# Kernel tuning notes

Measured on AMD Instinct MI355X. Metric: run time of the kernel, lower is better.

## Reference

```python
import jax, jax.numpy as jnp
import numpy as np

PI = float(np.pi)


def _m2(a, b, c, d):
    a, b, c, d = [jnp.asarray(x, jnp.complex64) for x in (a, b, c, d)]
    return jnp.stack([jnp.stack([a, b]), jnp.stack([c, d])])


def _rx(t):
    c, s = jnp.cos(t / 2), jnp.sin(t / 2)
    return _m2(c, -1j * s, -1j * s, c)


def _ry(t):
    c, s = jnp.cos(t / 2), jnp.sin(t / 2)
    return _m2(c, -s, s, c)


def _rz(t):
    e = jnp.exp(-0.5j * t)
    return _m2(e, 0.0, 0.0, jnp.conj(e))


def _rot(phi, theta, omega):
    # PennyLane Rot = RZ(omega) RY(theta) RZ(phi)
    return _rz(omega) @ _ry(theta) @ _rz(phi)


def _cgate(U):
    return jnp.eye(4, dtype=jnp.complex64).at[2:, 2:].set(U)


def _apply(state, U, wires):
    # state: [B] + [2]*8, U: [2^k, 2^k], wires: static wire indices
    axes = tuple(w + 1 for w in wires)
    k = len(wires)
    st = jnp.moveaxis(state, axes, tuple(range(1, 1 + k)))
    sh = st.shape
    st = jnp.einsum('ij,bjr->bir', U, st.reshape(sh[0], 2 ** k, -1))
    return jnp.moveaxis(st.reshape(sh), tuple(range(1, 1 + k)), axes)


def _mlp(x, W1, b1, W2, b2):
    return jax.nn.leaky_relu(x @ W1 + b1) @ W2 + b2


def _circuit(ang, inits, update):
    # ang: [B,7,2] = (RY,RZ) angles for wires 0..6 (edges on 0..2, nodes on 3..6); ancilla wire 7 = |0>
    a, b = ang[..., 0], ang[..., 1]
    q = jnp.stack([jnp.exp(-0.5j * b) * jnp.cos(0.5 * a),
                   jnp.exp(0.5j * b) * jnp.sin(0.5 * a)], -1).astype(jnp.complex64)  # [B,7,2]
    state = q[:, 0]
    for w in range(1, 7):
        state = jnp.einsum('b...,bk->b...k', state, q[:, w])
    state = jnp.einsum('b...,k->b...k', state, jnp.array([1.0, 0.0], jnp.complex64))  # [B]+[2]*8
    crx = _cgate(_rx(inits[0, 0]))
    cry = _cgate(_ry(inits[0, 1]))
    crz = _cgate(_rz(inits[0, 2]))
    for i in range(3):  # message_passing_pqc per edge
        state = _apply(state, crx, (4 + i, 7))
        state = _apply(state, cry, (i, 7))
        state = _apply(state, crz, (4 + i, 7))
    CNOT = jnp.array([[1, 0, 0, 0], [0, 1, 0, 0], [0, 0, 0, 1], [0, 0, 1, 0]], jnp.complex64)
    wgt = update[0]  # [L,2,3] StronglyEntanglingLayers on wires (3,7)
    for l in range(wgt.shape[0]):
        state = _apply(state, _rot(wgt[l, 0, 0], wgt[l, 0, 1], wgt[l, 0, 2]), (3,))
        state = _apply(state, _rot(wgt[l, 1, 0], wgt[l, 1, 1], wgt[l, 1, 2]), (7,))
        state = _apply(state, CNOT, (3, 7))
        state = _apply(state, CNOT, (7, 3))
    pr = state.real ** 2 + state.imag ** 2
    # probs over wires (3,7): sum out wires 0,1,2,4,5,6 -> [B,2,2] -> [B,4]
    return pr.sum(axis=(1, 2, 3, 5, 6, 7)).reshape(pr.shape[0], 4)


def setup_inputs() -> dict:
    N, DEG, NG = 32768, 3, 32
    FN, FE, H, PQC, POUT = 16, 8, 128, 2, 4
    rng = np.random.default_rng(0)
    f32 = lambda a: jnp.asarray(a, jnp.float32)
    p = lambda *s: f32(0.1 * rng.standard_normal(s))
    neighbors = rng.integers(0, N, size=(N, DEG))
    return dict(
        node_feat=f32(rng.standard_normal((N, FN))),
        edge_attr=f32(rng.standard_normal((N * DEG, FE))),
        node_W1=p(FN, H), node_b1=p(H), node_W2=p(H, PQC), node_b2=p(PQC),
        edge_W1=p(FE, H), edge_b1=p(H), edge_W2=p(H, PQC), edge_b2=p(PQC),
        inits=p(1, 3), update=p(1, 1, 2, 3),
        upd_W1=p(PQC + POUT, H), upd_b1=p(H), upd_W2=p(H, PQC), upd_b2=p(PQC),
        ln_g=jnp.ones((PQC,), jnp.float32), ln_b=jnp.zeros((PQC,), jnp.float32),
        head_W1=p(PQC, 2), head_b1=p(2), head_W2=p(2, 2), head_b2=p(2),
        sub_nodes=jnp.asarray(np.concatenate([np.arange(N)[:, None], neighbors], 1), jnp.int32),
        sub_edges=jnp.asarray(np.arange(N * DEG).reshape(N, DEG), jnp.int32),
        batch=jnp.asarray(np.arange(N) // (N // NG), jnp.int32),
    )


def reference(node_feat, edge_attr, node_W1, node_b1, node_W2, node_b2,
              edge_W1, edge_b1, edge_W2, edge_b2, inits, update,
              upd_W1, upd_b1, upd_W2, upd_b2, ln_g, ln_b,
              head_W1, head_b1, head_W2, head_b2,
              sub_nodes, sub_edges, batch):
    nf = jnp.tanh(_mlp(node_feat, node_W1, node_b1, node_W2, node_b2)) * PI  # [N,2]
    ef = jnp.tanh(_mlp(edge_attr, edge_W1, edge_b1, edge_W2, edge_b2)) * PI  # [E,2]
    ang = jnp.concatenate([ef[sub_edges], nf[sub_nodes]], axis=1)  # [N,7,2]
    probs = _circuit(ang, inits, update)  # [N,4]
    centers = sub_nodes[:, 0]
    upd = jnp.tanh(_mlp(jnp.concatenate([nf[centers], probs], 1),
                        upd_W1, upd_b1, upd_W2, upd_b2)) * PI
    updates_node = nf.at[centers].set((nf[centers] + upd) * 0.5)
    x = updates_node + nf
    mu = x.mean(-1, keepdims=True)
    var = ((x - mu) ** 2).mean(-1, keepdims=True)
    xn = (x - mu) / jnp.sqrt(var + 1e-5) * ln_g + ln_b  # LayerNorm(2)
    ng = 32
    g = jax.ops.segment_sum(xn, batch, num_segments=ng) / \
        jax.ops.segment_sum(jnp.ones_like(xn[:, :1]), batch, num_segments=ng)
    return _mlp(g, head_W1, head_b1, head_W2, head_b2)
```

## Files before the change

kernel.cpp:

```cpp
#include <hip/hip_runtime.h>
#include <math.h>

static constexpr float PI_F = 3.14159265358979323846f;


__device__ inline void rot2(float p, float t, float o, float R[2][2][2]) {
    float ct = cosf(0.5f*t), st = sinf(0.5f*t);
    float apo = 0.5f*(p+o), amo = 0.5f*(p-o);
    R[0][0][0] =  ct*cosf(apo); R[0][0][1] = -ct*sinf(apo);
    R[0][1][0] = -st*cosf(amo); R[0][1][1] = -st*sinf(amo);
    R[1][0][0] =  st*cosf(amo); R[1][0][1] = -st*sinf(amo);
    R[1][1][0] =  ct*cosf(apo); R[1][1][1] =  ct*sinf(apo);
}

__global__ __launch_bounds__(256) void k_mlp(
    const float* __restrict__ node_feat, const float* __restrict__ edge_attr,
    const float* __restrict__ nW1, const float* __restrict__ nb1,
    const float* __restrict__ nW2, const float* __restrict__ nb2,
    const float* __restrict__ eW1, const float* __restrict__ eb1,
    const float* __restrict__ eW2, const float* __restrict__ eb2,
    const float* __restrict__ inits, const float* __restrict__ update,
    float* __restrict__ ws, int N, int NE, int nbE)
{
    const int tid = threadIdx.x;
    const int blk = blockIdx.x;

    if (blk == 0) {
        if (tid < 96) ws[tid] = 0.f;
        if (tid == 96) ((int*)ws)[96] = 0;
        if (tid < 64) {
            float cx = cosf(0.5f*inits[0]), sx = sinf(0.5f*inits[0]);
            float cy = cosf(0.5f*inits[1]), sy = sinf(0.5f*inits[1]);
            float cz = cosf(0.5f*inits[2]), sz = sinf(0.5f*inits[2]);
            float v0r = 1.f, v0i = 0.f, v1r = 0.f, v1i = 0.f;
            #pragma unroll
            for (int i = 0; i < 3; ++i) {
                int xb = (tid >> (3+i)) & 1;
                int yb = (tid >> i) & 1;
                if (xb) {
                    float n0r = cx*v0r + sx*v1i, n0i = cx*v0i - sx*v1r;
                    float n1r = sx*v0i + cx*v1r, n1i = -sx*v0r + cx*v1i;
                    v0r=n0r; v0i=n0i; v1r=n1r; v1i=n1i;
                }
                if (yb) {
                    float n0r = cy*v0r - sy*v1r, n0i = cy*v0i - sy*v1i;
                    float n1r = sy*v0r + cy*v1r, n1i = sy*v0i + cy*v1i;
                    v0r=n0r; v0i=n0i; v1r=n1r; v1i=n1i;
                }
                if (xb) {
                    float n0r = cz*v0r + sz*v0i, n0i = cz*v0i - sz*v0r;
                    float n1r = cz*v1r - sz*v1i, n1i = cz*v1i + sz*v1r;
                    v0r=n0r; v0i=n0i; v1r=n1r; v1i=n1i;
                }
            }
            ws[128 + tid*4 + 0] = v0r*v0r + v0i*v0i;
            ws[128 + tid*4 + 1] = v1r*v1r + v1i*v1i;
            ws[128 + tid*4 + 2] = v0r*v1r + v0i*v1i;
            ws[128 + tid*4 + 3] = v0i*v1r - v0r*v1i;
        } else if (tid == 64) {
            float Ra[2][2][2], Rb[2][2][2];
            rot2(update[0], update[1], update[2], Ra);
            rot2(update[3], update[4], update[5], Rb);
            const int src[4] = {0, 2, 3, 1};
            #pragma unroll
            for (int k = 0; k < 4; ++k) {
                int r = src[k], r3 = r >> 1, r7 = r & 1;
                #pragma unroll
                for (int c = 0; c < 4; ++c) {
                    int c3 = c >> 1, c7 = c & 1;
                    float ar = Ra[r3][c3][0], ai = Ra[r3][c3][1];
                    float br = Rb[r7][c7][0], bi = Rb[r7][c7][1];
                    ws[384 + (k*4+c)*2 + 0] = ar*br - ai*bi;
                    ws[384 + (k*4+c)*2 + 1] = ar*bi + ai*br;
                }
            }
        }
    }

    if (blk < nbE) {
        int e = blk * 256 + tid;
        if (e >= NE) return;
        const float4* xp = (const float4*)(edge_attr + (size_t)e * 8);
        float4 v0 = xp[0], v1 = xp[1];
        float x[8] = {v0.x,v0.y,v0.z,v0.w, v1.x,v1.y,v1.z,v1.w};
        float t[128];
        #pragma unroll
        for (int h = 0; h < 128; ++h) t[h] = eb1[h];
        #pragma unroll
        for (int i = 0; i < 8; ++i) {
            const float* row = eW1 + i*128;
            float xi = x[i];
            #pragma unroll
            for (int h = 0; h < 128; ++h) t[h] = fmaf(xi, row[h], t[h]);
        }
        float acc = 0.f;
        #pragma unroll
        for (int h = 0; h < 128; ++h) {
            float lt = t[h] > 0.f ? t[h] : 0.01f * t[h];
            acc = fmaf(lt, eW2[2*h], acc);
        }
        ws[512 + 2*(size_t)N + e] = tanhf(acc + eb2[0]) * PI_F;
    } else {
        int n = (blk - nbE) * 256 + tid;
        if (n >= N) return;
        const float4* xp = (const float4*)(node_feat + (size_t)n * 16);
        float4 v0 = xp[0], v1 = xp[1], v2 = xp[2], v3 = xp[3];
        float x[16] = {v0.x,v0.y,v0.z,v0.w, v1.x,v1.y,v1.z,v1.w,
                       v2.x,v2.y,v2.z,v2.w, v3.x,v3.y,v3.z,v3.w};
        float t[128];
        #pragma unroll
        for (int h = 0; h < 128; ++h) t[h] = nb1[h];
        #pragma unroll
        for (int i = 0; i < 16; ++i) {
            const float* row = nW1 + i*128;
            float xi = x[i];
            #pragma unroll
            for (int h = 0; h < 128; ++h) t[h] = fmaf(xi, row[h], t[h]);
        }
        float a0 = 0.f, a1 = 0.f;
        #pragma unroll
        for (int h = 0; h < 128; ++h) {
            float lt = t[h] > 0.f ? t[h] : 0.01f * t[h];
            a0 = fmaf(lt, nW2[2*h],   a0);
            a1 = fmaf(lt, nW2[2*h+1], a1);
        }
        float2 o;
        o.x = tanhf(a0 + nb2[0]) * PI_F;
        o.y = tanhf(a1 + nb2[1]) * PI_F;
        ((float2*)(ws + 512))[n] = o;
    }
}

__global__ __launch_bounds__(256) void k_circ(
    float* __restrict__ ws,
    const float* __restrict__ uW1, const float* __restrict__ ub1,
    const float* __restrict__ uW2, const float* __restrict__ ub2,
    const float* __restrict__ lng, const float* __restrict__ lnb,
    const int* __restrict__ sub_nodes, const int* __restrict__ sub_edges,
    const int* __restrict__ batch,
    const float* __restrict__ hW1, const float* __restrict__ hb1,
    const float* __restrict__ hW2, const float* __restrict__ hb2,
    float* __restrict__ out, int N)
{
    const int tid = threadIdx.x;
    const float2* nf  = (const float2*)(ws + 512);
    const float* ef1  = ws + 512 + 2*(size_t)N;
    const float4* phi4 = (const float4*)(ws + 128);
    const float* U    = ws + 384;

    int n0 = blockIdx.x * 256 + tid;
    bool valid = n0 < N;
    int n = valid ? n0 : N - 1;

    const int4 sn = ((const int4*)sub_nodes)[n];
    int se0 = sub_edges[3*(size_t)n+0], se1 = sub_edges[3*(size_t)n+1], se2 = sub_edges[3*(size_t)n+2];

    float pe[3][2], pn[3][2];
    {
        float c0 = cosf(ef1[se0]), c1 = cosf(ef1[se1]), c2 = cosf(ef1[se2]);
        pe[0][0]=0.5f*(1.f+c0); pe[0][1]=0.5f*(1.f-c0);
        pe[1][0]=0.5f*(1.f+c1); pe[1][1]=0.5f*(1.f-c1);
        pe[2][0]=0.5f*(1.f+c2); pe[2][1]=0.5f*(1.f-c2);
        float d0 = cosf(nf[sn.y].x), d1 = cosf(nf[sn.z].x), d2 = cosf(nf[sn.w].x);
        pn[0][0]=0.5f*(1.f+d0); pn[0][1]=0.5f*(1.f-d0);
        pn[1][0]=0.5f*(1.f+d1); pn[1][1]=0.5f*(1.f-d1);
        pn[2][0]=0.5f*(1.f+d2); pn[2][1]=0.5f*(1.f-d2);
    }
    float E[8], Nw[8];
    #pragma unroll
    for (int m = 0; m < 8; ++m) {
        E[m]  = pe[0][m&1] * pe[1][(m>>1)&1] * pe[2][(m>>2)&1];
        Nw[m] = pn[0][m&1] * pn[1][(m>>1)&1] * pn[2][(m>>2)&1];
    }
    float S0 = 0.f, S1 = 0.f, Sr = 0.f, Si = 0.f;
    #pragma unroll
    for (int m = 0; m < 64; ++m) {
        float W = E[m & 7] * Nw[m >> 3];
        float4 g = phi4[m];
        S0 = fmaf(W, g.x, S0); S1 = fmaf(W, g.y, S1);
        Sr = fmaf(W, g.z, Sr); Si = fmaf(W, g.w, Si);
    }
    float2 nfc = nf[sn.x];
    float ca = cosf(0.5f*nfc.x), sa = sinf(0.5f*nfc.x);
    float cb = cosf(0.5f*nfc.y), sb = sinf(0.5f*nfc.y);
    float q0r = ca*cb, q0i = -ca*sb, q1r = sa*cb, q1i = sa*sb;
    float P[4];
    #pragma unroll
    for (int k = 0; k < 4; ++k) {
        float T0r, T0i, T1r, T1i;
        {
            float u0r = U[(k*4+0)*2], u0i = U[(k*4+0)*2+1];
            float u1r = U[(k*4+2)*2], u1i = U[(k*4+2)*2+1];
            T0r = u0r*q0r - u0i*q0i + u1r*q1r - u1i*q1i;
            T0i = u0r*q0i + u0i*q0r + u1r*q1i + u1i*q1r;
        }
        {
            float u0r = U[(k*4+1)*2], u0i = U[(k*4+1)*2+1];
            float u1r = U[(k*4+3)*2], u1i = U[(k*4+3)*2+1];
            T1r = u0r*q0r - u0i*q0i + u1r*q1r - u1i*q1i;
            T1i = u0r*q0i + u0i*q0r + u1r*q1i + u1i*q1r;
        }
        float Ar = T0r*T1r + T0i*T1i, Ai = T0i*T1r - T0r*T1i;
        P[k] = (T0r*T0r + T0i*T0i)*S0 + (T1r*T1r + T1i*T1i)*S1 + 2.f*(Ar*Sr - Ai*Si);
    }
    float in6[6] = {nfc.x, nfc.y, P[0], P[1], P[2], P[3]};
    float t[128];
    #pragma unroll
    for (int h = 0; h < 128; ++h) t[h] = ub1[h];
    #pragma unroll
    for (int i = 0; i < 6; ++i) {
        const float* row = uW1 + i*128;
        float xi = in6[i];
        #pragma unroll
        for (int h = 0; h < 128; ++h) t[h] = fmaf(xi, row[h], t[h]);
    }
    float u0 = 0.f, u1 = 0.f;
    #pragma unroll
    for (int h = 0; h < 128; ++h) {
        float lt = t[h] > 0.f ? t[h] : 0.01f * t[h];
        u0 = fmaf(lt, uW2[2*h],   u0);
        u1 = fmaf(lt, uW2[2*h+1], u1);
    }
    float x0 = 1.5f*nfc.x + 0.5f*(tanhf(u0 + ub2[0]) * PI_F);
    float x1 = 1.5f*nfc.y + 0.5f*(tanhf(u1 + ub2[1]) * PI_F);
    float mu = 0.5f*(x0 + x1);
    float d  = x0 - mu;
    float inv = 1.0f / sqrtf(d*d + 1e-5f);
    float wv  = valid ? 1.f : 0.f;
    float xn0 = ( d*inv*lng[0] + lnb[0]) * wv;
    float xn1 = (-d*inv*lng[1] + lnb[1]) * wv;
    int bs = batch[n];

    bool uni = __all(bs == __shfl(bs, 0));
    if (uni) {
        float r0 = xn0, r1 = xn1, rc = wv;
        #pragma unroll
        for (int off = 32; off >= 1; off >>= 1) {
            r0 += __shfl_xor(r0, off); r1 += __shfl_xor(r1, off); rc += __shfl_xor(rc, off);
        }
        if ((tid & 63) == 0) {
            atomicAdd(&ws[bs*3+0], r0);
            atomicAdd(&ws[bs*3+1], r1);
            atomicAdd(&ws[bs*3+2], rc);
        }
    } else if (valid) {
        atomicAdd(&ws[bs*3+0], xn0);
        atomicAdd(&ws[bs*3+1], xn1);
        atomicAdd(&ws[bs*3+2], 1.f);
    }

    __shared__ int sLast;
    __threadfence();
    __syncthreads();
    if (tid == 0) {
        int old = atomicAdd((int*)ws + 96, 1);
        sLast = (old == (int)gridDim.x - 1) ? 1 : 0;
    }
    __syncthreads();
    if (sLast && tid < 32) {
        float cnt = atomicAdd(&ws[tid*3+2], 0.f);
        float iv  = cnt > 0.f ? 1.f/cnt : 0.f;
        float g0  = atomicAdd(&ws[tid*3+0], 0.f) * iv;
        float g1  = atomicAdd(&ws[tid*3+1], 0.f) * iv;
        float h0, h1;
        {
            float a = hb1[0] + g0*hW1[0] + g1*hW1[2];
            float b = hb1[1] + g0*hW1[1] + g1*hW1[3];
            h0 = a > 0.f ? a : 0.01f*a;
            h1 = b > 0.f ? b : 0.01f*b;
        }
        out[tid*2+0] = hb2[0] + h0*hW2[0] + h1*hW2[2];
        out[tid*2+1] = hb2[1] + h0*hW2[1] + h1*hW2[3];
    }
}

extern "C" void kernel_launch(void* const* d_in, const int* in_sizes, int n_in,
                              void* d_out, int out_size, void* d_ws, size_t ws_size,
                              hipStream_t stream)
{
    const float* node_feat = (const float*)d_in[0];
    const float* edge_attr = (const float*)d_in[1];
    const float* node_W1 = (const float*)d_in[2];
    const float* node_b1 = (const float*)d_in[3];
    const float* node_W2 = (const float*)d_in[4];
    const float* node_b2 = (const float*)d_in[5];
    const float* edge_W1 = (const float*)d_in[6];
    const float* edge_b1 = (const float*)d_in[7];
    const float* edge_W2 = (const float*)d_in[8];
    const float* edge_b2 = (const float*)d_in[9];
    const float* inits   = (const float*)d_in[10];
    const float* update  = (const float*)d_in[11];
    const float* upd_W1  = (const float*)d_in[12];
    const float* upd_b1  = (const float*)d_in[13];
    const float* upd_W2  = (const float*)d_in[14];
    const float* upd_b2  = (const float*)d_in[15];
    const float* ln_g    = (const float*)d_in[16];
    const float* ln_b    = (const float*)d_in[17];
    const float* head_W1 = (const float*)d_in[18];
    const float* head_b1 = (const float*)d_in[19];
    const float* head_W2 = (const float*)d_in[20];
    const float* head_b2 = (const float*)d_in[21];
    const int* sub_nodes = (const int*)d_in[22];
    const int* sub_edges = (const int*)d_in[23];
    const int* batch     = (const int*)d_in[24];

    int N  = in_sizes[24];
    int NE = in_sizes[1] / 8;

    float* w = (float*)d_ws;
    size_t need = (512 + 2*(size_t)N + (size_t)NE) * sizeof(float);
    if (ws_size < need) return;

    int nbE = (NE + 255) / 256;
    int nbN = (N + 255) / 256;
    k_mlp<<<nbE + nbN, 256, 0, stream>>>(node_feat, edge_attr,
        node_W1, node_b1, node_W2, node_b2,
        edge_W1, edge_b1, edge_W2, edge_b2,
        inits, update, w, N, NE, nbE);
    k_circ<<<nbN, 256, 0, stream>>>(w,
        upd_W1, upd_b1, upd_W2, upd_b2, ln_g, ln_b,
        sub_nodes, sub_edges, batch,
        head_W1, head_b1, head_W2, head_b2,
        (float*)d_out, N);
}
```

Measured before the change: 44.43 us.

## Pre-transpose MLP weights into per-hidden-unit rows and loop over hidden units

Adds a prep kernel that repacks the node, edge and update MLP weights into per-hidden-unit rows with the bias and output weights interleaved. Each MLP is then computed one hidden unit at a time using float4 loads, so the 128-float register array of hidden activations is no longer needed. The intent is lower register pressure, better occupancy and fewer scalar loads. The cost is an extra kernel launch on the serial path and a larger workspace.

```diff
diff --git a/kernel.cpp b/kernel.cpp
--- a/kernel.cpp
+++ b/kernel.cpp
@@ -3,6 +3,10 @@
 
 static constexpr float PI_F = 3.14159265358979323846f;
 
+#define WS_NT 448
+#define WS_ET 3008
+#define WS_UT 4544
+#define WS_NF 6144
 
 __device__ inline void rot2(float p, float t, float o, float R[2][2][2]) {
     float ct = cosf(0.5f*t), st = sinf(0.5f*t);
@@ -13,128 +17,149 @@
     R[1][1][0] =  ct*cosf(apo); R[1][1][1] =  ct*sinf(apo);
 }
 
+__global__ __launch_bounds__(256) void k_prep(
+    const float* __restrict__ nW1, const float* __restrict__ nb1, const float* __restrict__ nW2,
+    const float* __restrict__ eW1, const float* __restrict__ eb1, const float* __restrict__ eW2,
+    const float* __restrict__ uW1, const float* __restrict__ ub1, const float* __restrict__ uW2,
+    const float* __restrict__ inits, const float* __restrict__ update,
+    float* __restrict__ ws)
+{
+    const int tid = threadIdx.x;
+    if (tid < 96) ws[tid] = 0.f;
+    if (tid == 96) ((int*)ws)[96] = 0;
+
+    if (tid < 64) {
+        float cx = cosf(0.5f*inits[0]), sx = sinf(0.5f*inits[0]);
+        float cy = cosf(0.5f*inits[1]), sy = sinf(0.5f*inits[1]);
+        float cz = cosf(0.5f*inits[2]), sz = sinf(0.5f*inits[2]);
+        float v0r = 1.f, v0i = 0.f, v1r = 0.f, v1i = 0.f;
+        #pragma unroll
+        for (int i = 0; i < 3; ++i) {
+            int xb = (tid >> (3+i)) & 1;
+            int yb = (tid >> i) & 1;
+            if (xb) {
+                float n0r = cx*v0r + sx*v1i, n0i = cx*v0i - sx*v1r;
+                float n1r = sx*v0i + cx*v1r, n1i = -sx*v0r + cx*v1i;
+                v0r=n0r; v0i=n0i; v1r=n1r; v1i=n1i;
+            }
+            if (yb) {
+                float n0r = cy*v0r - sy*v1r, n0i = cy*v0i - sy*v1i;
+                float n1r = sy*v0r + cy*v1r, n1i = sy*v0i + cy*v1i;
+                v0r=n0r; v0i=n0i; v1r=n1r; v1i=n1i;
+            }
+            if (xb) {
+                float n0r = cz*v0r + sz*v0i, n0i = cz*v0i - sz*v0r;
+                float n1r = cz*v1r - sz*v1i, n1i = cz*v1i + sz*v1r;
+                v0r=n0r; v0i=n0i; v1r=n1r; v1i=n1i;
+            }
+        }
+        ws[128 + tid*4 + 0] = v0r*v0r + v0i*v0i;
+        ws[128 + tid*4 + 1] = v1r*v1r + v1i*v1i;
+        ws[128 + tid*4 + 2] = v0r*v1r + v0i*v1i;
+        ws[128 + tid*4 + 3] = v0i*v1r - v0r*v1i;
+    } else if (tid == 64) {
+        float Ra[2][2][2], Rb[2][2][2];
+        rot2(update[0], update[1], update[2], Ra);
+        rot2(update[3], update[4], update[5], Rb);
+        const int src[4] = {0, 2, 3, 1};
+        #pragma unroll
+        for (int k = 0; k < 4; ++k) {
+            int r = src[k], r3 = r >> 1, r7 = r & 1;
+            #pragma unroll
+            for (int c = 0; c < 4; ++c) {
+                int c3 = c >> 1, c7 = c & 1;
+                float ar = Ra[r3][c3][0], ai = Ra[r3][c3][1];
+                float br = Rb[r7][c7][0], bi = Rb[r7][c7][1];
+                ws[384 + (k*4+c)*2 + 0] = ar*br - ai*bi;
+                ws[384 + (k*4+c)*2 + 1] = ar*bi + ai*br;
+            }
+        }
+    }
+
+    if (tid < 128) {
+        int h = tid;
+        float* r = ws + WS_NT + h*20;
+        #pragma unroll
+        for (int i = 0; i < 16; ++i) r[i] = nW1[i*128 + h];
+        r[16] = nb1[h]; r[17] = nW2[2*h]; r[18] = nW2[2*h+1]; r[19] = 0.f;
+    } else {
+        int h = tid - 128;
+        float* re = ws + WS_ET + h*12;
+        #pragma unroll
+        for (int i = 0; i < 8; ++i) re[i] = eW1[i*128 + h];
+        re[8] = eb1[h]; re[9] = eW2[2*h]; re[10] = 0.f; re[11] = 0.f;
+        float* ru = ws + WS_UT + h*12;
+        #pragma unroll
+        for (int i = 0; i < 6; ++i) ru[i] = uW1[i*128 + h];
+        ru[6] = ub1[h]; ru[7] = uW2[2*h]; ru[8] = uW2[2*h+1];
+        ru[9] = 0.f; ru[10] = 0.f; ru[11] = 0.f;
+    }
+}
+
 __global__ __launch_bounds__(256) void k_mlp(
     const float* __restrict__ node_feat, const float* __restrict__ edge_attr,
-    const float* __restrict__ nW1, const float* __restrict__ nb1,
-    const float* __restrict__ nW2, const float* __restrict__ nb2,
-    const float* __restrict__ eW1, const float* __restrict__ eb1,
-    const float* __restrict__ eW2, const float* __restrict__ eb2,
-    const float* __restrict__ inits, const float* __restrict__ update,
-    float* __restrict__ ws, int N, int NE, int nbE)
+    const float* __restrict__ nT, const float* __restrict__ eT,
+    const float* __restrict__ nb2, const float* __restrict__ eb2,
+    float2* __restrict__ nf, float* __restrict__ ef1,
+    int N, int NE, int nbE)
 {
     const int tid = threadIdx.x;
     const int blk = blockIdx.x;
-
-    if (blk == 0) {
-        if (tid < 96) ws[tid] = 0.f;
-        if (tid == 96) ((int*)ws)[96] = 0;
-        if (tid < 64) {
-            float cx = cosf(0.5f*inits[0]), sx = sinf(0.5f*inits[0]);
-            float cy = cosf(0.5f*inits[1]), sy = sinf(0.5f*inits[1]);
-            float cz = cosf(0.5f*inits[2]), sz = sinf(0.5f*inits[2]);
-            float v0r = 1.f, v0i = 0.f, v1r = 0.f, v1i = 0.f;
-            #pragma unroll
-            for (int i = 0; i < 3; ++i) {
-                int xb = (tid >> (3+i)) & 1;
-                int yb = (tid >> i) & 1;
-                if (xb) {
-                    float n0r = cx*v0r + sx*v1i, n0i = cx*v0i - sx*v1r;
-                    float n1r = sx*v0i + cx*v1r, n1i = -sx*v0r + cx*v1i;
-                    v0r=n0r; v0i=n0i; v1r=n1r; v1i=n1i;
-                }
-                if (yb) {
-                    float n0r = cy*v0r - sy*v1r, n0i = cy*v0i - sy*v1i;
-                    float n1r = sy*v0r + cy*v1r, n1i = sy*v0i + cy*v1i;
-                    v0r=n0r; v0i=n0i; v1r=n1r; v1i=n1i;
-                }
-                if (xb) {
-                    float n0r = cz*v0r + sz*v0i, n0i = cz*v0i - sz*v0r;
-                    float n1r = cz*v1r - sz*v1i, n1i = cz*v1i + sz*v1r;
-                    v0r=n0r; v0i=n0i; v1r=n1r; v1i=n1i;
-                }
-            }
-            ws[128 + tid*4 + 0] = v0r*v0r + v0i*v0i;
-            ws[128 + tid*4 + 1] = v1r*v1r + v1i*v1i;
-            ws[128 + tid*4 + 2] = v0r*v1r + v0i*v1i;
-            ws[128 + tid*4 + 3] = v0i*v1r - v0r*v1i;
-        } else if (tid == 64) {
-            float Ra[2][2][2], Rb[2][2][2];
-            rot2(update[0], update[1], update[2], Ra);
-            rot2(update[3], update[4], update[5], Rb);
-            const int src[4] = {0, 2, 3, 1};
-            #pragma unroll
-            for (int k = 0; k < 4; ++k) {
-                int r = src[k], r3 = r >> 1, r7 = r & 1;
-                #pragma unroll
-                for (int c = 0; c < 4; ++c) {
-                    int c3 = c >> 1, c7 = c & 1;
-                    float ar = Ra[r3][c3][0], ai = Ra[r3][c3][1];
-                    float br = Rb[r7][c7][0], bi = Rb[r7][c7][1];
-                    ws[384 + (k*4+c)*2 + 0] = ar*br - ai*bi;
-                    ws[384 + (k*4+c)*2 + 1] = ar*bi + ai*br;
-                }
-            }
-        }
-    }
 
     if (blk < nbE) {
         int e = blk * 256 + tid;
         if (e >= NE) return;
         const float4* xp = (const float4*)(edge_attr + (size_t)e * 8);
-        float4 v0 = xp[0], v1 = xp[1];
-        float x[8] = {v0.x,v0.y,v0.z,v0.w, v1.x,v1.y,v1.z,v1.w};
-        float t[128];
-        #pragma unroll
-        for (int h = 0; h < 128; ++h) t[h] = eb1[h];
-        #pragma unroll
-        for (int i = 0; i < 8; ++i) {
-            const float* row = eW1 + i*128;
-            float xi = x[i];
-            #pragma unroll
-            for (int h = 0; h < 128; ++h) t[h] = fmaf(xi, row[h], t[h]);
-        }
+        float4 xv0 = xp[0], xv1 = xp[1];
         float acc = 0.f;
-        #pragma unroll
+        #pragma unroll 4
         for (int h = 0; h < 128; ++h) {
-            float lt = t[h] > 0.f ? t[h] : 0.01f * t[h];
-            acc = fmaf(lt, eW2[2*h], acc);
-        }
-        ws[512 + 2*(size_t)N + e] = tanhf(acc + eb2[0]) * PI_F;
+            const float4* r = (const float4*)(eT + h*12);
+            float4 f0 = r[0], f1 = r[1], f2 = r[2];
+            float t = f2.x;
+            t = fmaf(xv0.x, f0.x, t); t = fmaf(xv0.y, f0.y, t);
+            t = fmaf(xv0.z, f0.z, t); t = fmaf(xv0.w, f0.w, t);
+            t = fmaf(xv1.x, f1.x, t); t = fmaf(xv1.y, f1.y, t);
+            t = fmaf(xv1.z, f1.z, t); t = fmaf(xv1.w, f1.w, t);
+            float lt = t > 0.f ? t : 0.01f * t;
+            acc = fmaf(lt, f2.y, acc);
+        }
+        ef1[e] = tanhf(acc + eb2[0]) * PI_F;
     } else {
         int n = (blk - nbE) * 256 + tid;
         if (n >= N) return;
         const float4* xp = (const float4*)(node_feat + (size_t)n * 16);
-        float4 v0 = xp[0], v1 = xp[1], v2 = xp[2], v3 = xp[3];
-        float x[16] = {v0.x,v0.y,v0.z,v0.w, v1.x,v1.y,v1.z,v1.w,
-                       v2.x,v2.y,v2.z,v2.w, v3.x,v3.y,v3.z,v3.w};
-        float t[128];
-        #pragma unroll
-        for (int h = 0; h < 128; ++h) t[h] = nb1[h];
-        #pragma unroll
-        for (int i = 0; i < 16; ++i) {
-            const float* row = nW1 + i*128;
-            float xi = x[i];
-            #pragma unroll
-            for (int h = 0; h < 128; ++h) t[h] = fmaf(xi, row[h], t[h]);
-        }
+        float4 xv0 = xp[0], xv1 = xp[1], xv2 = xp[2], xv3 = xp[3];
         float a0 = 0.f, a1 = 0.f;
-        #pragma unroll
+        #pragma unroll 4
         for (int h = 0; h < 128; ++h) {
-            float lt = t[h] > 0.f ? t[h] : 0.01f * t[h];
-            a0 = fmaf(lt, nW2[2*h],   a0);
-            a1 = fmaf(lt, nW2[2*h+1], a1);
+            const float4* r = (const float4*)(nT + h*20);
+            float4 f0 = r[0], f1 = r[1], f2 = r[2], f3 = r[3], f4 = r[4];
+            float t = f4.x;
+            t = fmaf(xv0.x, f0.x, t); t = fmaf(xv0.y, f0.y, t);
+            t = fmaf(xv0.z, f0.z, t); t = fmaf(xv0.w, f0.w, t);
+            t = fmaf(xv1.x, f1.x, t); t = fmaf(xv1.y, f1.y, t);
+            t = fmaf(xv1.z, f1.z, t); t = fmaf(xv1.w, f1.w, t);
+            t = fmaf(xv2.x, f2.x, t); t = fmaf(xv2.y, f2.y, t);
+            t = fmaf(xv2.z, f2.z, t); t = fmaf(xv2.w, f2.w, t);
+            t = fmaf(xv3.x, f3.x, t); t = fmaf(xv3.y, f3.y, t);
+            t = fmaf(xv3.z, f3.z, t); t = fmaf(xv3.w, f3.w, t);
+            float lt = t > 0.f ? t : 0.01f * t;
+            a0 = fmaf(lt, f4.y, a0);
+            a1 = fmaf(lt, f4.z, a1);
         }
         float2 o;
         o.x = tanhf(a0 + nb2[0]) * PI_F;
         o.y = tanhf(a1 + nb2[1]) * PI_F;
-        ((float2*)(ws + 512))[n] = o;
+        nf[n] = o;
     }
 }
 
 __global__ __launch_bounds__(256) void k_circ(
     float* __restrict__ ws,
-    const float* __restrict__ uW1, const float* __restrict__ ub1,
-    const float* __restrict__ uW2, const float* __restrict__ ub2,
+    const float4* __restrict__ phi4, const float* __restrict__ U,
+    const float* __restrict__ uT, const float* __restrict__ ub2,
+    const float2* __restrict__ nf, const float* __restrict__ ef1,
     const float* __restrict__ lng, const float* __restrict__ lnb,
     const int* __restrict__ sub_nodes, const int* __restrict__ sub_edges,
     const int* __restrict__ batch,
@@ -143,11 +168,6 @@
     float* __restrict__ out, int N)
 {
     const int tid = threadIdx.x;
-    const float2* nf  = (const float2*)(ws + 512);
-    const float* ef1  = ws + 512 + 2*(size_t)N;
-    const float4* phi4 = (const float4*)(ws + 128);
-    const float* U    = ws + 384;
-
     int n0 = blockIdx.x * 256 + tid;
     bool valid = n0 < N;
     int n = valid ? n0 : N - 1;
@@ -187,39 +207,29 @@
     float P[4];
     #pragma unroll
     for (int k = 0; k < 4; ++k) {
-        float T0r, T0i, T1r, T1i;
-        {
-            float u0r = U[(k*4+0)*2], u0i = U[(k*4+0)*2+1];
-            float u1r = U[(k*4+2)*2], u1i = U[(k*4+2)*2+1];
-            T0r = u0r*q0r - u0i*q0i + u1r*q1r - u1i*q1i;
-            T0i = u0r*q0i + u0i*q0r + u1r*q1i + u1i*q1r;
-        }
-        {
-            float u0r = U[(k*4+1)*2], u0i = U[(k*4+1)*2+1];
-            float u1r = U[(k*4+3)*2], u1i = U[(k*4+3)*2+1];
-            T1r = u0r*q0r - u0i*q0i + u1r*q1r - u1i*q1i;
-            T1i = u0r*q0i + u0i*q0r + u1r*q1i + u1i*q1r;
-        }
+        float u0r = U[(k*4+0)*2], u0i = U[(k*4+0)*2+1];
+        float u1r = U[(k*4+2)*2], u1i = U[(k*4+2)*2+1];
+        float T0r = u0r*q0r - u0i*q0i + u1r*q1r - u1i*q1i;
+        float T0i = u0r*q0i + u0i*q0r + u1r*q1i + u1i*q1r;
+        float v0r_ = U[(k*4+1)*2], v0i_ = U[(k*4+1)*2+1];
+        float v1r_ = U[(k*4+3)*2], v1i_ = U[(k*4+3)*2+1];
+        float T1r = v0r_*q0r - v0i_*q0i + v1r_*q1r - v1i_*q1i;
+        float T1i = v0r_*q0i + v0i_*q0r + v1r_*q1i + v1i_*q1r;
         float Ar = T0r*T1r + T0i*T1i, Ai = T0i*T1r - T0r*T1i;
         P[k] = (T0r*T0r + T0i*T0i)*S0 + (T1r*T1r + T1i*T1i)*S1 + 2.f*(Ar*Sr - Ai*Si);
     }
-    float in6[6] = {nfc.x, nfc.y, P[0], P[1], P[2], P[3]};
-    float t[128];
-    #pragma unroll
-    for (int h = 0; h < 128; ++h) t[h] = ub1[h];
-    #pragma unroll
-    for (int i = 0; i < 6; ++i) {
-        const float* row = uW1 + i*128;
-        float xi = in6[i];
-        #pragma unroll
-        for (int h = 0; h < 128; ++h) t[h] = fmaf(xi, row[h], t[h]);
-    }
     float u0 = 0.f, u1 = 0.f;
-    #pragma unroll
+    #pragma unroll 4
     for (int h = 0; h < 128; ++h) {
-        float lt = t[h] > 0.f ? t[h] : 0.01f * t[h];
-        u0 = fmaf(lt, uW2[2*h],   u0);
-        u1 = fmaf(lt, uW2[2*h+1], u1);
+        const float4* r = (const float4*)(uT + h*12);
+        float4 f0 = r[0], f1 = r[1], f2 = r[2];
+        float t = f1.z;
+        t = fmaf(nfc.x, f0.x, t); t = fmaf(nfc.y, f0.y, t);
+        t = fmaf(P[0],  f0.z, t); t = fmaf(P[1],  f0.w, t);
+        t = fmaf(P[2],  f1.x, t); t = fmaf(P[3],  f1.y, t);
+        float lt = t > 0.f ? t : 0.01f * t;
+        u0 = fmaf(lt, f1.w, u0);
+        u1 = fmaf(lt, f2.x, u1);
     }
     float x0 = 1.5f*nfc.x + 0.5f*(tanhf(u0 + ub2[0]) * PI_F);
     float x1 = 1.5f*nfc.y + 0.5f*(tanhf(u1 + ub2[1]) * PI_F);
@@ -262,13 +272,10 @@
         float iv  = cnt > 0.f ? 1.f/cnt : 0.f;
         float g0  = atomicAdd(&ws[tid*3+0], 0.f) * iv;
         float g1  = atomicAdd(&ws[tid*3+1], 0.f) * iv;
-        float h0, h1;
-        {
-            float a = hb1[0] + g0*hW1[0] + g1*hW1[2];
-            float b = hb1[1] + g0*hW1[1] + g1*hW1[3];
-            h0 = a > 0.f ? a : 0.01f*a;
-            h1 = b > 0.f ? b : 0.01f*b;
-        }
+        float a = hb1[0] + g0*hW1[0] + g1*hW1[2];
+        float b = hb1[1] + g0*hW1[1] + g1*hW1[3];
+        float h0 = a > 0.f ? a : 0.01f*a;
+        float h1 = b > 0.f ? b : 0.01f*b;
         out[tid*2+0] = hb2[0] + h0*hW2[0] + h1*hW2[2];
         out[tid*2+1] = hb2[1] + h0*hW2[1] + h1*hW2[3];
     }
@@ -308,18 +315,24 @@
     int NE = in_sizes[1] / 8;
 
     float* w = (float*)d_ws;
-    size_t need = (512 + 2*(size_t)N + (size_t)NE) * sizeof(float);
+    size_t need = ((size_t)WS_NF + 2*(size_t)N + (size_t)NE) * sizeof(float);
     if (ws_size < need) return;
+
+    float2* nf = (float2*)(w + WS_NF);
+    float* ef1 = w + WS_NF + 2*(size_t)N;
 
     int nbE = (NE + 255) / 256;
     int nbN = (N + 255) / 256;
+
+    k_prep<<<1, 256, 0, stream>>>(node_W1, node_b1, node_W2,
+                                  edge_W1, edge_b1, edge_W2,
+                                  upd_W1, upd_b1, upd_W2,
+                                  inits, update, w);
     k_mlp<<<nbE + nbN, 256, 0, stream>>>(node_feat, edge_attr,
-        node_W1, node_b1, node_W2, node_b2,
-        edge_W1, edge_b1, edge_W2, edge_b2,
-        inits, update, w, N, NE, nbE);
+        w + WS_NT, w + WS_ET, node_b2, edge_b2, nf, ef1, N, NE, nbE);
     k_circ<<<nbN, 256, 0, stream>>>(w,
-        upd_W1, upd_b1, upd_W2, upd_b2, ln_g, ln_b,
-        sub_nodes, sub_edges, batch,
+        (const float4*)(w + 128), w + 384, w + WS_UT, upd_b2,
+        nf, ef1, ln_g, ln_b, sub_nodes, sub_edges, batch,
         head_W1, head_b1, head_W2, head_b2,
         (float*)d_out, N);
 }
```

Result: slower. 57.12 us (+28.6%).
